# Kernel tuning notes

Hardware: AMD Instinct MI355X
Metric: run time of the kernel (lower is better)

Reference implementation:

```python
import jax, jax.numpy as jnp
import numpy as np

B, C, H, W = 2, 72, 96, 96
FACTOR = 4  # input_dim // output_dim = 72 // 18


def setup_inputs() -> dict:
    key = jax.random.key(0)
    ks = jax.random.split(key, 7)
    s = 1.0 / np.sqrt(C)
    return {
        "x": jax.random.normal(ks[0], (B, C, H, W), dtype=jnp.float32),
        "Wq": jax.random.normal(ks[1], (C, C), dtype=jnp.float32) * s,
        "bq": jax.random.normal(ks[2], (C,), dtype=jnp.float32) * 0.01,
        "Wk": jax.random.normal(ks[3], (C, C), dtype=jnp.float32) * s,
        "bk": jax.random.normal(ks[4], (C,), dtype=jnp.float32) * 0.01,
        "Wv": jax.random.normal(ks[5], (C, C), dtype=jnp.float32) * s,
        "bv": jax.random.normal(ks[6], (C,), dtype=jnp.float32) * 0.01,
    }


def reference(x, Wq, bq, Wk, bk, Wv, bv):
    b, c, h, w = x.shape
    n = h * w
    flat = x.reshape(b, c, n)  # [B, C, N]
    # 1x1 convs == per-pixel channel matmuls
    q = jnp.einsum('dc,bcn->bdn', Wq, flat) + bq[None, :, None]
    k = jnp.einsum('dc,bcn->bdn', Wk, flat) + bk[None, :, None]
    v = jnp.einsum('dc,bcn->bdn', Wv, flat) + bv[None, :, None]
    # scores[b,i,j] = sum_c q[b,c,i] * k[b,c,j]  (no 1/sqrt(d) scaling, as in source)
    scores = jnp.einsum('bci,bcj->bij', q, k)  # [B, N, N]
    attn = jax.nn.softmax(scores, axis=-1)
    # weighted_values = bmm(v, attn^T): wv[b,c,i] = sum_j v[b,c,j] * attn[b,i,j]
    wv = jnp.einsum('bcj,bij->bci', v, attn)  # [B, C, N]
    wv = wv.reshape(b, c // FACTOR, FACTOR, h, w)
    xg = x.reshape(b, c // FACTOR, FACTOR, h, w)
    pooled = jnp.sum(xg * wv, axis=2)  # [B, C//FACTOR, H, W]
    return pooled
```

## Files before the change

### kernel.cpp

```cpp
#include <hip/hip_runtime.h>

#define NPIX 9216
#define CIN 72
#define CP 96
#define SPLITS 8
#define JCHUNK (NPIX / SPLITS)
#define JTILES (JCHUNK / 64)
#define L2E   1.44269504088896f
#define EXPB  46.1662413084468f

typedef __attribute__((ext_vector_type(8))) short bf16x8;
typedef __attribute__((ext_vector_type(8))) _Float16 f16x8;
typedef __attribute__((ext_vector_type(4))) float f32x4;

#define MFMA_BF16(A,B,C) __builtin_amdgcn_mfma_f32_16x16x32_bf16(A,B,C,0,0,0)
#define MFMA_F16(A,B,C)  __builtin_amdgcn_mfma_f32_16x16x32_f16(A,B,C,0,0,0)

static __device__ __forceinline__ unsigned short f2bf(float f) {
  unsigned u = __float_as_uint(f);
  u += 0x7fffu + ((u >> 16) & 1u);
  return (unsigned short)(u >> 16);
}
static __device__ __forceinline__ float bf2f(unsigned short h) {
  return __uint_as_float(((unsigned)h) << 16);
}
static __device__ __forceinline__ unsigned short f2h(float f) {
  _Float16 h = (_Float16)f;
  return *(unsigned short*)&h;
}
static __device__ __forceinline__ unsigned pack_bf_trunc(float lo, float hi) {
  return (__float_as_uint(lo) >> 16) | (__float_as_uint(hi) & 0xffff0000u);
}
static __device__ __forceinline__ void load_lds16(const void* g, void* l) {
  __builtin_amdgcn_global_load_lds(
      (const __attribute__((address_space(1))) unsigned int*)g,
      (__attribute__((address_space(3))) unsigned int*)l, 16, 0, 0);
}

__global__ __launch_bounds__(256) void wprep_kernel(
    const float* __restrict__ Wq, const float* __restrict__ Wk,
    const float* __restrict__ Wv,
    unsigned short* __restrict__ WH, unsigned short* __restrict__ WL)
{
  int id = blockIdx.x * 256 + threadIdx.x;
  if (id >= 3 * 80 * 96) return;
  int mat = id / (80 * 96);
  int rem = id % (80 * 96);
  int d = rem / 96, c = rem % 96;
  const float* W = (mat == 0) ? Wq : (mat == 1) ? Wk : Wv;
  float v = (d < 72 && c < 72) ? W[d * 72 + c] : 0.f;
  unsigned short hi = f2bf(v);
  WH[id] = hi;
  WL[id] = f2bf(v - bf2f(hi));
}

#define XTS 104
#define QS  4

static __device__ __forceinline__ void stage_x(const float* __restrict__ x,
    float* lbuf, int b, int n0, int w, int lane) {
#pragma unroll
  for (int kk = 0; kk < 2; ++kk) {
    const int ch = w * 2 + kk;
    const int r = ch * 16 + (lane >> 2);
    const int c = (r < 72) ? r : 71;
    const float* src = x + ((size_t)b * CIN + c) * NPIX + n0 + (lane & 3) * 4;
    load_lds16(src, lbuf + ch * 256);
  }
}

__global__ __launch_bounds__(192, 1) void qkv_kernel(
    const float* __restrict__ x,
    const unsigned short* __restrict__ WH, const unsigned short* __restrict__ WL,
    const float* __restrict__ bq, const float* __restrict__ bk,
    const float* __restrict__ bv,
    unsigned short* __restrict__ QH, unsigned short* __restrict__ KH,
    unsigned short* __restrict__ VG)
{
  __shared__ __align__(16) float ls_x[2][6 * 256];
  __shared__ __align__(16) unsigned short obuf[2][16 * XTS];

  const int t    = threadIdx.x;
  const int w    = t >> 6;
  const int lane = t & 63;
  const int quad = lane >> 4;
  const int l15  = lane & 15;
  const int bid  = blockIdx.x;
  const int b    = bid / 144;
  const int g0   = bid % 144;
  const int nbase = g0 * 64;

  const unsigned short* wh = WH + w * 80 * 96;
  const unsigned short* wl = WL + w * 80 * 96;
  bf16x8 WAh[5][3], WAl[5][3];
#pragma unroll
  for (int dm = 0; dm < 5; ++dm)
#pragma unroll
    for (int ks = 0; ks < 3; ++ks) {
      WAh[dm][ks] = *(const bf16x8*)(wh + (dm * 16 + l15) * 96 + ks * 32 + quad * 8);
      WAl[dm][ks] = *(const bf16x8*)(wl + (dm * 16 + l15) * 96 + ks * 32 + quad * 8);
    }
  const float* bias = (w == 0) ? bq : (w == 1) ? bk : bv;
  float bs[5][4];
#pragma unroll
  for (int dm = 0; dm < 5; ++dm)
#pragma unroll
    for (int r = 0; r < 4; ++r) {
      int d = dm * 16 + quad * 4 + r;
      bs[dm][r] = (d < 72) ? bias[d] : 0.f;
    }

  stage_x(x, ls_x[0], b, nbase, w, lane);
  __syncthreads();

  for (int s = 0; s < QS; ++s) {
    const int n0 = nbase + s * 16;
    if (s + 1 < QS) stage_x(x, ls_x[(s + 1) & 1], b, n0 + 16, w, lane);
    const float* lx = ls_x[s & 1];

    bf16x8 xbh[3], xbl[3];
#pragma unroll
    for (int ks = 0; ks < 3; ++ks) {
#pragma unroll
      for (int j = 0; j < 8; ++j) {
        float v = lx[(ks * 32 + quad * 8 + j) * 16 + l15];
        unsigned short hi = f2bf(v);
        ((unsigned short*)&xbh[ks])[j] = hi;
        ((unsigned short*)&xbl[ks])[j] = f2bf(v - bf2f(hi));
      }
    }

    f32x4 acc[5];
#pragma unroll
    for (int dm = 0; dm < 5; ++dm) {
      acc[dm] = (f32x4){0.f, 0.f, 0.f, 0.f};
#pragma unroll
      for (int ks = 0; ks < 3; ++ks) {
        acc[dm] = MFMA_BF16(WAh[dm][ks], xbh[ks], acc[dm]);
        acc[dm] = MFMA_BF16(WAh[dm][ks], xbl[ks], acc[dm]);
        acc[dm] = MFMA_BF16(WAl[dm][ks], xbh[ks], acc[dm]);
      }
    }

    if (w < 2) {
      unsigned short* ob = obuf[w];
#pragma unroll
      for (int dm = 0; dm < 5; ++dm)
#pragma unroll
        for (int r = 0; r < 4; ++r) {
          int d = dm * 16 + quad * 4 + r;
          float v = acc[dm][r] + bs[dm][r];
          ob[l15 * XTS + d] = f2h(v);
        }
      unsigned short* outp = (w == 0) ? QH : KH;
      const size_t obase = ((size_t)b * NPIX + n0) * CP;
      uint4 z; z.x = z.y = z.z = z.w = 0u;
      for (int f = lane; f < 192; f += 64) {
        int row = f / 12, col = f % 12;
        *(uint4*)(outp + obase + (size_t)row * CP + col * 8) =
            (col < 10) ? *(const uint4*)(ob + row * XTS + col * 8) : z;
      }
    } else {
#pragma unroll
      for (int dm = 0; dm < 5; ++dm)
#pragma unroll
        for (int r = 0; r < 4; ++r) {
          int d = dm * 16 + quad * 4 + r;
          float v = (d < 72) ? acc[dm][r] + bs[dm][r] : (d == 72 ? 1.0f : 0.f);
          VG[((size_t)b * 80 + d) * NPIX + n0 + l15] = f2bf(v);
        }
    }
    __syncthreads();
  }
}

#define KSP 128
#define VSP 72

__global__ __launch_bounds__(256, 3) void flash_kernel(
    const float* __restrict__ x,
    const unsigned short* __restrict__ QH, const unsigned short* __restrict__ KH,
    const unsigned short* __restrict__ VG,
    float* __restrict__ NUM, float* __restrict__ LPART)
{
  __shared__ __align__(16) unsigned short ls_kh[64 * KSP];
  __shared__ __align__(16) unsigned short ls_vs[80 * VSP];
  __shared__ __align__(16) unsigned short ps[4][48 * 64];

  const int t    = threadIdx.x;
  const int w    = t >> 6;
  const int lane = t & 63;
  const int quad = lane >> 4;
  const int l15  = lane & 15;

  const int bid  = blockIdx.x;
  const int sp   = bid & 7;
  const int slot = bid >> 3;
  const int b    = slot / 48;
  const int it   = slot % 48;
  const int i0w  = it * 192 + w * 48;

  f16x8 qh[3][3];
#pragma unroll
  for (int mi = 0; mi < 3; ++mi)
#pragma unroll
    for (int ks = 0; ks < 3; ++ks) {
      size_t off = ((size_t)b * NPIX + i0w + mi * 16 + l15) * CP + ks * 32 + quad * 8;
      qh[mi][ks] = *(const f16x8*)(QH + off);
    }

  f32x4 oacc[3][5];
#pragma unroll
  for (int mi = 0; mi < 3; ++mi)
#pragma unroll
    for (int nt = 0; nt < 5; ++nt) oacc[mi][nt] = (f32x4){0.f, 0.f, 0.f, 0.f};

  unsigned short* psw = ps[w];
  const int swz = l15 & 7;

  const unsigned short* kpg = KH + ((size_t)b * NPIX + sp * JCHUNK) * CP;
  const unsigned short* vpg = VG + (size_t)b * 80 * NPIX + sp * JCHUNK;

  for (int jt = 0; jt < JTILES; ++jt, kpg += 64 * CP, vpg += 64) {
#pragma unroll
    for (int k = 0; k < 4; ++k) {
      int chunk = w + k * 4;
      int r  = chunk * 4 + (lane >> 4);
      int lu = (lane & 15) ^ (r & 7);
      int su = (lu < 12) ? lu : 0;
      load_lds16(kpg + r * CP + su * 8, ls_kh + chunk * 512);
    }
    for (int idx = t; idx < 640; idx += 256) {
      int r = idx >> 3, c = idx & 7;
      *(uint4*)(ls_vs + r * VSP + c * 8) =
          *(const uint4*)(vpg + (size_t)r * NPIX + c * 8);
    }
    __syncthreads();

#pragma unroll
    for (int tj = 0; tj < 4; ++tj) {
      const int krow = tj * 16 + l15;
      f16x8 fkh[3];
#pragma unroll
      for (int ks = 0; ks < 3; ++ks)
        fkh[ks] = *(const f16x8*)(ls_kh + krow * KSP + (((ks * 4 + quad) ^ swz) << 3));
#pragma unroll
      for (int mi = 0; mi < 3; ++mi) {
        f32x4 s = (f32x4){0.f, 0.f, 0.f, 0.f};
        s = MFMA_F16(fkh[0], qh[mi][0], s);
        s = MFMA_F16(fkh[1], qh[mi][1], s);
        s = MFMA_F16(fkh[2], qh[mi][2], s);
        float p0 = __builtin_amdgcn_exp2f(__builtin_fmaf(s[0], L2E, -EXPB));
        float p1 = __builtin_amdgcn_exp2f(__builtin_fmaf(s[1], L2E, -EXPB));
        float p2 = __builtin_amdgcn_exp2f(__builtin_fmaf(s[2], L2E, -EXPB));
        float p3 = __builtin_amdgcn_exp2f(__builtin_fmaf(s[3], L2E, -EXPB));
        uint2 pk;
        pk.x = pack_bf_trunc(p0, p1);
        pk.y = pack_bf_trunc(p2, p3);
        int pu = (tj * 2 + (quad >> 1)) ^ swz;
        *(uint2*)(psw + (mi * 16 + l15) * 64 + (pu << 3) + (quad & 1) * 4) = pk;
      }
    }

#pragma unroll
    for (int js = 0; js < 2; ++js) {
      bf16x8 pf[3];
#pragma unroll
      for (int mi = 0; mi < 3; ++mi)
        pf[mi] = *(const bf16x8*)(psw + (mi * 16 + l15) * 64 +
                                  ((((js << 2) + quad) ^ swz) << 3));
#pragma unroll
      for (int nt = 0; nt < 5; ++nt) {
        bf16x8 vf = *(const bf16x8*)(ls_vs + (nt * 16 + l15) * VSP + js * 32 + quad * 8);
#pragma unroll
        for (int mi = 0; mi < 3; ++mi)
          oacc[mi][nt] = MFMA_BF16(vf, pf[mi], oacc[mi][nt]);
      }
    }
    __syncthreads();
  }

  const size_t sb = (size_t)(sp * 2 + b);
#pragma unroll
  for (int mi = 0; mi < 3; ++mi) {
    const int i = i0w + mi * 16 + l15;
    if (quad == 2)
      LPART[sb * NPIX + i] = oacc[mi][4][0];
#pragma unroll
    for (int nt = 0; nt < 5; ++nt) {
      int c0 = nt * 16 + quad * 4;
      if (c0 < 72) {
        float num = 0.f;
#pragma unroll
        for (int r = 0; r < 4; ++r)
          num = __builtin_fmaf(x[((size_t)b * CIN + c0 + r) * NPIX + i],
                               oacc[mi][nt][r], num);
        NUM[(sb * 18 + (c0 >> 2)) * NPIX + i] = num;
      }
    }
  }
}

__global__ __launch_bounds__(256) void combine_pool_kernel(
    const float* __restrict__ NUM, const float* __restrict__ LPART,
    float* __restrict__ out)
{
  int id = blockIdx.x * 256 + threadIdx.x;
  if (id >= 2 * 18 * (NPIX / 4)) return;
  int n = (id % (NPIX / 4)) * 4;
  int rest = id / (NPIX / 4);
  int g = rest % 18, b = rest / 18;

  float4 A = make_float4(0.f, 0.f, 0.f, 0.f);
  float4 L = make_float4(0.f, 0.f, 0.f, 0.f);
#pragma unroll
  for (int s = 0; s < SPLITS; ++s) {
    size_t sb = (size_t)(s * 2 + b);
    float4 a = *(const float4*)(NUM + (sb * 18 + g) * NPIX + n);
    float4 l = *(const float4*)(LPART + sb * NPIX + n);
    A.x += a.x; A.y += a.y; A.z += a.z; A.w += a.w;
    L.x += l.x; L.y += l.y; L.z += l.z; L.w += l.w;
  }
  float4 r;
  r.x = A.x / L.x; r.y = A.y / L.y; r.z = A.z / L.z; r.w = A.w / L.w;
  *(float4*)(out + (size_t)id * 4) = r;
}

extern "C" void kernel_launch(void* const* d_in, const int* in_sizes, int n_in,
                              void* d_out, int out_size, void* d_ws, size_t ws_size,
                              hipStream_t stream) {
  const float* x  = (const float*)d_in[0];
  const float* Wq = (const float*)d_in[1];
  const float* bq = (const float*)d_in[2];
  const float* Wk = (const float*)d_in[3];
  const float* bk = (const float*)d_in[4];
  const float* Wv = (const float*)d_in[5];
  const float* bv = (const float*)d_in[6];
  float* out = (float*)d_out;

  char* p = (char*)d_ws;
  const size_t szQK = (size_t)2 * NPIX * CP * 2;
  unsigned short* QH = (unsigned short*)p; p += szQK;
  unsigned short* KH = (unsigned short*)p; p += szQK;
  unsigned short* VG = (unsigned short*)p; p += (size_t)2 * 80 * NPIX * 2;
  unsigned short* WH = (unsigned short*)p; p += (size_t)3 * 80 * 96 * 2;
  unsigned short* WL = (unsigned short*)p; p += (size_t)3 * 80 * 96 * 2;
  float* NUM = (float*)p; p += (size_t)SPLITS * 2 * 18 * NPIX * 4;
  float* LPART = (float*)p; p += (size_t)SPLITS * 2 * NPIX * 4;

  wprep_kernel<<<(3 * 80 * 96 + 255) / 256, 256, 0, stream>>>(Wq, Wk, Wv, WH, WL);
  qkv_kernel<<<288, 192, 0, stream>>>(x, WH, WL, bq, bk, bv, QH, KH, VG);
  flash_kernel<<<768, 256, 0, stream>>>(x, QH, KH, VG, NUM, LPART);
  combine_pool_kernel<<<(2 * 18 * (NPIX / 4) + 255) / 256, 256, 0, stream>>>(
      NUM, LPART, out);
}
```

Baseline: 150.7 us.

## Store K, V and P tiles in LDS in MFMA fragment order

Changes the shared-memory layout of the K, V and probability tiles so each 512-element chunk holds one 16x32 MFMA operand fragment in lane order. Fragment reads become contiguous lane*8 loads with no XOR swizzle. V is now loaded through the direct-to-LDS path like K, instead of a register round-trip through uint4 loads and stores. Global loads per lane still gather 16-byte rows across strided addresses, and the unpadded contiguous layout trades the swizzle for linear per-lane access.

```diff
diff --git a/kernel.cpp b/kernel.cpp
--- a/kernel.cpp
+++ b/kernel.cpp
@@ -174,8 +174,8 @@
   }
 }
 
-#define KSP 128
-#define VSP 72
+#define KCH 12
+#define VCH 10
 
 __global__ __launch_bounds__(256, 3) void flash_kernel(
     const float* __restrict__ x,
@@ -183,9 +183,9 @@
     const unsigned short* __restrict__ VG,
     float* __restrict__ NUM, float* __restrict__ LPART)
 {
-  __shared__ __align__(16) unsigned short ls_kh[64 * KSP];
-  __shared__ __align__(16) unsigned short ls_vs[80 * VSP];
-  __shared__ __align__(16) unsigned short ps[4][48 * 64];
+  __shared__ __align__(16) unsigned short ls_kh[KCH * 512];
+  __shared__ __align__(16) unsigned short ls_vs[VCH * 512];
+  __shared__ __align__(16) unsigned short ps[4][6 * 512];
 
   const int t    = threadIdx.x;
   const int w    = t >> 6;
@@ -216,34 +216,35 @@
     for (int nt = 0; nt < 5; ++nt) oacc[mi][nt] = (f32x4){0.f, 0.f, 0.f, 0.f};
 
   unsigned short* psw = ps[w];
-  const int swz = l15 & 7;
 
   const unsigned short* kpg = KH + ((size_t)b * NPIX + sp * JCHUNK) * CP;
   const unsigned short* vpg = VG + (size_t)b * 80 * NPIX + sp * JCHUNK;
 
+  int koff[3], voff[3];
+#pragma unroll
+  for (int k = 0; k < 3; ++k) {
+    int c = w + 4 * k;
+    koff[k] = ((c / 3) * 16 + l15) * CP + (c % 3) * 32 + quad * 8;
+    int cv = (c < VCH) ? c : 0;
+    voff[k] = ((cv >> 1) * 16 + l15) * NPIX + (cv & 1) * 32 + quad * 8;
+  }
+
   for (int jt = 0; jt < JTILES; ++jt, kpg += 64 * CP, vpg += 64) {
 #pragma unroll
-    for (int k = 0; k < 4; ++k) {
-      int chunk = w + k * 4;
-      int r  = chunk * 4 + (lane >> 4);
-      int lu = (lane & 15) ^ (r & 7);
-      int su = (lu < 12) ? lu : 0;
-      load_lds16(kpg + r * CP + su * 8, ls_kh + chunk * 512);
-    }
-    for (int idx = t; idx < 640; idx += 256) {
-      int r = idx >> 3, c = idx & 7;
-      *(uint4*)(ls_vs + r * VSP + c * 8) =
-          *(const uint4*)(vpg + (size_t)r * NPIX + c * 8);
-    }
+    for (int k = 0; k < 3; ++k)
+      load_lds16(kpg + koff[k], ls_kh + (w + 4 * k) * 512);
+#pragma unroll
+    for (int k = 0; k < 3; ++k)
+      if (w + 4 * k < VCH)
+        load_lds16(vpg + voff[k], ls_vs + (w + 4 * k) * 512);
     __syncthreads();
 
 #pragma unroll
     for (int tj = 0; tj < 4; ++tj) {
-      const int krow = tj * 16 + l15;
       f16x8 fkh[3];
 #pragma unroll
       for (int ks = 0; ks < 3; ++ks)
-        fkh[ks] = *(const f16x8*)(ls_kh + krow * KSP + (((ks * 4 + quad) ^ swz) << 3));
+        fkh[ks] = *(const f16x8*)(ls_kh + (tj * 3 + ks) * 512 + lane * 8);
 #pragma unroll
       for (int mi = 0; mi < 3; ++mi) {
         f32x4 s = (f32x4){0.f, 0.f, 0.f, 0.f};
@@ -257,8 +258,9 @@
         uint2 pk;
         pk.x = pack_bf_trunc(p0, p1);
         pk.y = pack_bf_trunc(p2, p3);
-        int pu = (tj * 2 + (quad >> 1)) ^ swz;
-        *(uint2*)(psw + (mi * 16 + l15) * 64 + (pu << 3) + (quad & 1) * 4) = pk;
+        int qq = (tj & 1) * 2 + (quad >> 1);
+        *(uint2*)(psw + (mi * 2 + (tj >> 1)) * 512 + qq * 128 + l15 * 8 +
+                  (quad & 1) * 4) = pk;
       }
     }
 
@@ -267,11 +269,10 @@
       bf16x8 pf[3];
 #pragma unroll
       for (int mi = 0; mi < 3; ++mi)
-        pf[mi] = *(const bf16x8*)(psw + (mi * 16 + l15) * 64 +
-                                  ((((js << 2) + quad) ^ swz) << 3));
+        pf[mi] = *(const bf16x8*)(psw + (mi * 2 + js) * 512 + lane * 8);
 #pragma unroll
       for (int nt = 0; nt < 5; ++nt) {
-        bf16x8 vf = *(const bf16x8*)(ls_vs + (nt * 16 + l15) * VSP + js * 32 + quad * 8);
+        bf16x8 vf = *(const bf16x8*)(ls_vs + (nt * 2 + js) * 512 + lane * 8);
 #pragma unroll
         for (int mi = 0; mi < 3; ++mi)
           oacc[mi][nt] = MFMA_BF16(vf, pf[mi], oacc[mi][nt]);
```

New measurement: 148.9 us. No clear change (-1.2%).
